# Kernel optimization log

Hardware: AMD Instinct MI355X
Metric: run time of the kernel (lower is better)

Reference implementation:

```python
import jax, jax.numpy as jnp
import numpy as np

EPS = 1e-9       # module's displacement/convergence epsilon
COS_EPS = 1e-8   # torch F.cosine_similarity eps (norms clamped at eps)
LN_EPS = 1e-5


def _safe_norm(sq):
    # sqrt with zero-safe gradient for exactly-zero (padded) vectors
    return jnp.where(sq > 0, jnp.sqrt(jnp.maximum(sq, 1e-30)), 0.0)


def _features(coords, n):
    """coords: [S, md] padded; n: true length (>=4). Returns [60] features."""
    S, md = coords.shape
    f32 = coords.dtype
    nf = n.astype(f32)
    idx_d = jnp.arange(S - 1)
    m = n - 1                       # number of valid deltas
    mf = m.astype(f32)
    dmask = idx_d < m
    dmaskf = dmask.astype(f32)

    deltas = (coords[1:] - coords[:-1]) * dmaskf[:, None]     # [S-1, md]
    dmags = _safe_norm(jnp.sum(deltas * deltas, axis=-1))      # [S-1]

    last = jnp.take(coords, n - 1, axis=0)
    total_disp = _safe_norm(jnp.sum((last - coords[0]) ** 2))
    path_len = jnp.sum(dmags)
    disp_ratio = total_disp / (path_len + EPS)
    n_steps_norm = nf / 10.0

    # consecutive cosine similarities / curvatures (valid count = n-2)
    na = jnp.maximum(dmags, COS_EPS)
    cos = jnp.sum(deltas[:-1] * deltas[1:], axis=-1) / (na[:-1] * na[1:])  # [S-2]
    idx_c = jnp.arange(S - 2)
    cmask = idx_c < (n - 2)
    cmaskf = cmask.astype(f32)
    ncf = (n - 2).astype(f32)
    curv = 1.0 - cos
    curv_m = jnp.where(cmask, curv, 0.0)
    mean_curv = jnp.sum(curv_m) / ncf
    max_curv = jnp.max(jnp.where(cmask, curv, -jnp.inf))
    min_curv = jnp.min(jnp.where(cmask, curv, jnp.inf))
    curv_var = jnp.sum(cmaskf * (curv - mean_curv) ** 2) / jnp.maximum(ncf - 1.0, 1.0)
    std_curv = jnp.where(ncf > 1.0, jnp.sqrt(jnp.maximum(curv_var, 1e-30)), 0.0)
    curv_range = max_curv - min_curv

    mean_cos = jnp.sum(jnp.where(cmask, cos, 0.0)) / ncf
    min_cos = jnp.min(jnp.where(cmask, cos, jnp.inf))
    dir_changes = jnp.sum(cmaskf * (cos < 0).astype(f32)) / jnp.maximum(ncf, 1.0)

    linearity = disp_ratio
    loop_score = 1.0 - total_disp / (path_len + EPS)

    half = m // 2
    fmaskf = (idx_d < half + 1).astype(f32)
    smaskf = ((idx_d >= half) & (idx_d < m)).astype(f32)
    first_half = jnp.sum(dmags * fmaskf) / (half + 1).astype(f32)
    second_half = jnp.sum(dmags * smaskf) / (m - half).astype(f32)
    convergence = (first_half - second_half) / (first_half + EPS)
    cascade = (second_half - first_half) / (first_half + EPS)

    # all-pairs cosine (the O(n^2) block) via one GEMM per sample
    cosmat = (deltas @ deltas.T) / (na[:, None] * na[None, :])  # [S-1, S-1]
    pmask = (idx_d[:, None] < idx_d[None, :]) & (idx_d[None, :] < m)
    npairs = mf * (mf - 1.0) / 2.0
    parallelism = jnp.sum(jnp.where(pmask, cosmat, 0.0)) / jnp.maximum(npairs, 1.0)

    mean_dm = path_len / mf
    dm_var = jnp.sum(dmaskf * (dmags - mean_dm) ** 2) / jnp.maximum(mf - 1.0, 1.0)
    std_dm = jnp.where(mf > 1.0, jnp.sqrt(jnp.maximum(dm_var, 1e-30)), 0.0)
    max_dm = jnp.max(jnp.where(dmask, dmags, -jnp.inf))
    jump = jnp.where(mean_dm > EPS, max_dm / mean_dm, 1.0)

    rmaskf = (jnp.arange(S) < n).astype(f32)
    cnt = nf * md
    mean_coord = jnp.sum(coords * rmaskf[:, None]) / cnt
    coord_var = jnp.sum(rmaskf[:, None] * (coords - mean_coord) ** 2) / (cnt - 1.0)
    std_coord = jnp.sqrt(jnp.maximum(coord_var, 1e-30))

    scalars = jnp.stack([
        total_disp, path_len, disp_ratio, n_steps_norm,
        mean_curv, max_curv, std_curv, curv_range,
        mean_cos, min_cos, dir_changes,
        linearity, loop_score, convergence, parallelism, jump, cascade,
        mean_dm, std_dm, mean_coord, std_coord,
    ])  # [21]
    padded_deltas = deltas[:3].reshape(-1)   # [30] (masked -> already zero-padded)
    padded_curvs = curv_m[:9]                # [9]
    return jnp.concatenate([scalars, padded_deltas, padded_curvs])  # [60]


def setup_inputs() -> dict:
    key = jax.random.key(0)
    ks = jax.random.split(key, 4)
    B, S, md, H = 32768, 48, 10, 48
    coords = jax.random.normal(ks[0], (B, S, md), dtype=jnp.float32)
    lengths = jax.random.randint(ks[1], (B,), 4, S + 1, dtype=jnp.int32)
    W = jax.random.normal(ks[2], (60, H), dtype=jnp.float32) * 0.1
    b = jax.random.normal(ks[3], (H,), dtype=jnp.float32) * 0.01
    ln_w = jnp.ones((H,), dtype=jnp.float32)
    ln_b = jnp.zeros((H,), dtype=jnp.float32)
    return {"coords": coords, "lengths": lengths, "W": W, "b": b, "ln_w": ln_w, "ln_b": ln_b}


def reference(coords, lengths, W, b, ln_w, ln_b):
    feats = jax.vmap(_features)(coords, lengths)          # [B, 60]
    h = feats @ W + b                                     # [B, 48]
    mu = jnp.mean(h, axis=-1, keepdims=True)
    var = jnp.mean((h - mu) ** 2, axis=-1, keepdims=True)
    h = (h - mu) / jnp.sqrt(var + LN_EPS) * ln_w + ln_b
    return jax.nn.gelu(h, approximate=False)              # dropout is identity at eval
```

## Files before the change

### kernel.cpp

```cpp
#include <hip/hip_runtime.h>
#include <math.h>

#define WPB 4

static __device__ __forceinline__ float frcp(float x){ return __builtin_amdgcn_rcpf(x); }
static __device__ __forceinline__ float fsq (float x){ return __builtin_amdgcn_sqrtf(x); }
static __device__ __forceinline__ float rld(float x, int l){
  return __uint_as_float(__builtin_amdgcn_readlane(__float_as_uint(x), l));
}

template<int CTRL, int RM>
static __device__ __forceinline__ float dppadd(float x){
  int t = __builtin_amdgcn_update_dpp(0, __float_as_int(x), CTRL, RM, 0xf, true);
  return x + __int_as_float(t);
}
template<int CTRL, int RM>
static __device__ __forceinline__ float dppmax(float x){
  int t = __builtin_amdgcn_update_dpp(__float_as_int(x), __float_as_int(x), CTRL, RM, 0xf, false);
  return fmaxf(x, __int_as_float(t));
}
template<int CTRL, int RM>
static __device__ __forceinline__ float dppmin(float x){
  int t = __builtin_amdgcn_update_dpp(__float_as_int(x), __float_as_int(x), CTRL, RM, 0xf, false);
  return fminf(x, __int_as_float(t));
}
static __device__ __forceinline__ float wsum63(float x){
  x = dppadd<0x111,0xf>(x); x = dppadd<0x112,0xf>(x);
  x = dppadd<0x114,0xf>(x); x = dppadd<0x118,0xf>(x);
  x = dppadd<0x142,0xa>(x); x = dppadd<0x143,0xc>(x);
  return x;
}
static __device__ __forceinline__ float wmax63(float x){
  x = dppmax<0x111,0xf>(x); x = dppmax<0x112,0xf>(x);
  x = dppmax<0x114,0xf>(x); x = dppmax<0x118,0xf>(x);
  x = dppmax<0x142,0xa>(x); x = dppmax<0x143,0xc>(x);
  return x;
}
static __device__ __forceinline__ float wmin63(float x){
  x = dppmin<0x111,0xf>(x); x = dppmin<0x112,0xf>(x);
  x = dppmin<0x114,0xf>(x); x = dppmin<0x118,0xf>(x);
  x = dppmin<0x142,0xa>(x); x = dppmin<0x143,0xc>(x);
  return x;
}

__global__ void transpose_w(const float* __restrict__ W, float* __restrict__ Wt){
  int idx = blockIdx.x * 256 + threadIdx.x;
  if (idx < 60 * 48) { int f = idx / 48, j = idx - f * 48; Wt[j * 60 + f] = W[idx]; }
}

template<bool USEWT>
__global__ __launch_bounds__(WPB * 64)
void traj_kernel(const float* __restrict__ coords,
                 const int* __restrict__ lengths,
                 const float* __restrict__ Wsrc,
                 const float* __restrict__ bias,
                 const float* __restrict__ lnw,
                 const float* __restrict__ lnb,
                 float* __restrict__ out, int B)
{
  const int i = threadIdx.x & 63;
  const int b = blockIdx.x * WPB + (threadIdx.x >> 6);
  if (b >= B) return;

  const int n = __builtin_amdgcn_readfirstlane(lengths[b]);
  const int m = n - 1;
  const int half = m >> 1;
  const float* cp = coords + (size_t)b * 480;

  const int r0 = (i < 47) ? i : 47;
  const int r1 = (i + 1 < 47) ? (i + 1) : 47;
  const int r2 = (i + 2 < 47) ? (i + 2) : 47;
  float c[10], cn[10], cnn[10];
  {
    const float2* p = reinterpret_cast<const float2*>(cp + r0 * 10);
#pragma unroll
    for (int k = 0; k < 5; ++k){ float2 v = p[k]; c[2*k]=v.x; c[2*k+1]=v.y; }
    p = reinterpret_cast<const float2*>(cp + r1 * 10);
#pragma unroll
    for (int k = 0; k < 5; ++k){ float2 v = p[k]; cn[2*k]=v.x; cn[2*k+1]=v.y; }
    p = reinterpret_cast<const float2*>(cp + r2 * 10);
#pragma unroll
    for (int k = 0; k < 5; ++k){ float2 v = p[k]; cnn[2*k]=v.x; cnn[2*k+1]=v.y; }
  }

  float d[10], dn[10];
  float dsq = 0.f, dsqn = 0.f, dot = 0.f;
#pragma unroll
  for (int k = 0; k < 10; ++k) {
    float a = cn[k] - c[k];   d[k]  = a;  dsq  = fmaf(a, a, dsq);
    float e = cnn[k] - cn[k]; dn[k] = e;  dsqn = fmaf(e, e, dsqn);
    dot = fmaf(a, e, dot);
  }
  const float sn   = (dsq  > 0.f) ? fsq(fmaxf(dsq,  1e-30f)) : 0.f;
  const float snn  = (dsqn > 0.f) ? fsq(fmaxf(dsqn, 1e-30f)) : 0.f;
  const float inv  = frcp(fmaxf(sn,  1e-8f));
  const float invn = frcp(fmaxf(snn, 1e-8f));

  const bool dact = (i < m);
  const float dm  = dact ? sn  : 0.f;
  const bool cact = (i < n - 2);
  const float cosv   = dot * inv * invn;
  const float cm     = cact ? cosv : 0.f;
  const float curv_m = cact ? (1.f - cosv) : 0.f;

  float csl = 0.f, cs2l = 0.f;
#pragma unroll
  for (int k = 0; k < 10; ++k) { csl += c[k]; cs2l = fmaf(c[k], c[k], cs2l); }
  const bool ract = (i < n);
  csl  = ract ? csl  : 0.f;
  cs2l = ract ? cs2l : 0.f;

  float tql = 0.f;
#pragma unroll
  for (int k = 0; k < 10; ++k) {
    float t = c[k] - rld(c[k], 0);
    tql = fmaf(t, t, tql);
  }
  const float tsq = rld(tql, m);
  const float total_disp = (tsq > 0.f) ? fsq(fmaxf(tsq, 1e-30f)) : 0.f;

  const float path_len = wsum63(dm);
  const float sum_dm2  = wsum63(dact ? dsq : 0.f);
  const float max_dm   = wmax63(dm);
  const float sum_f    = wsum63((i <= half) ? dm : 0.f);
  const float dm_half  = rld(dm, half);
  const float sum_cos  = wsum63(cm);
  const float sum_cos2 = wsum63(cm * cm);
  const float max_cos  = wmax63(cact ? cosv : -INFINITY);
  const float min_cos  = wmin63(cact ? cosv :  INFINITY);
  const float sum_ng   = wsum63((cact && cosv < 0.f) ? 1.f : 0.f);
  const float sum_c    = wsum63(csl);
  const float sum_c2   = wsum63(cs2l);
  const float invm = dact ? inv : 0.f;
  float Usq = 0.f;
#pragma unroll
  for (int k = 0; k < 10; ++k) {
    float Uk = wsum63(d[k] * invm);
    Usq = fmaf(Uk, Uk, Usq);
  }
  const float sum_uu = wsum63(dsq * invm * invm);

  const float EPSf = 1e-9f;
  const float nf = (float)n, mf = (float)m, ncf = (float)(n - 2);
  const float rncf = frcp(ncf);
  const float sum_s = path_len + dm_half - sum_f;
  const float disp_ratio = total_disp * frcp(path_len + EPSf);
  const float mean_cv = (ncf - sum_cos) * rncf;
  const float sum_cv2 = fmaf(-2.f, sum_cos, ncf) + sum_cos2;
  const float cv_var  = (sum_cv2 - ncf * mean_cv * mean_cv) * frcp(fmaxf(ncf - 1.f, 1.f));
  const float std_cv  = fsq(fmaxf(cv_var, 1e-30f));
  const float fh = sum_f * frcp((float)(half + 1));
  const float sh = sum_s * frcp((float)(m - half));
  const float conv = (fh - sh) * frcp(fh + EPSf);
  const float npairs = mf * (mf - 1.f) * 0.5f;
  const float par = (Usq - sum_uu) * 0.5f * frcp(npairs);
  const float mean_dm = path_len * frcp(mf);
  const float dm_var = (sum_dm2 - mf * mean_dm * mean_dm) * frcp(mf - 1.f);
  const float std_dm = fsq(fmaxf(dm_var, 1e-30f));
  const float jump = (mean_dm > EPSf) ? max_dm * frcp(mean_dm) : 1.f;
  const float cnt = nf * 10.f;
  const float mean_co = sum_c * frcp(cnt);
  const float co_var = (sum_c2 - cnt * mean_co * mean_co) * frcp(cnt - 1.f);
  const float std_co = fsq(fmaxf(co_var, 1e-30f));

  float feat[60];
  feat[0]  = rld(total_disp, 63);
  feat[1]  = rld(path_len, 63);
  feat[2]  = rld(disp_ratio, 63);
  feat[3]  = nf * 0.1f;
  feat[4]  = rld(mean_cv, 63);
  feat[5]  = 1.f - rld(min_cos, 63);
  feat[6]  = rld(std_cv, 63);
  feat[7]  = rld(max_cos - min_cos, 63);
  feat[8]  = rld(sum_cos * rncf, 63);
  feat[9]  = rld(min_cos, 63);
  feat[10] = rld(sum_ng * rncf, 63);
  feat[11] = feat[2];
  feat[12] = 1.f - feat[2];
  feat[13] = rld(conv, 63);
  feat[14] = rld(par, 63);
  feat[15] = rld(jump, 63);
  feat[16] = -feat[13];
  feat[17] = rld(mean_dm, 63);
  feat[18] = rld(std_dm, 63);
  feat[19] = rld(mean_co, 63);
  feat[20] = rld(std_co, 63);
#pragma unroll
  for (int k = 0; k < 10; ++k) feat[21 + k] = rld(d[k], 0);
#pragma unroll
  for (int k = 0; k < 10; ++k) feat[31 + k] = rld(d[k], 1);
#pragma unroll
  for (int k = 0; k < 10; ++k) feat[41 + k] = rld(d[k], 2);
#pragma unroll
  for (int r = 0; r < 9; ++r)  feat[51 + r] = rld(curv_m, r);

  const int jc = (i < 48) ? i : 47;
  float h = bias[jc];
  if (USEWT) {
    const float4* wr = reinterpret_cast<const float4*>(Wsrc + jc * 60);
#pragma unroll
    for (int t = 0; t < 15; ++t) {
      float4 w = wr[t];
      h = fmaf(feat[4*t+0], w.x, h);
      h = fmaf(feat[4*t+1], w.y, h);
      h = fmaf(feat[4*t+2], w.z, h);
      h = fmaf(feat[4*t+3], w.w, h);
    }
  } else {
#pragma unroll
    for (int f = 0; f < 60; ++f) h = fmaf(feat[f], Wsrc[f * 48 + jc], h);
  }

  const float hm = (i < 48) ? h : 0.f;
  const float s1 = rld(wsum63(hm), 63);
  const float s2 = rld(wsum63(hm * hm), 63);
  const float mu  = s1 * (1.f / 48.f);
  const float var = fmaf(-mu, mu, s2 * (1.f / 48.f));
  const float rstd = __builtin_amdgcn_rsqf(var + 1e-5f);

  if (i < 48) {
    float x = (h - mu) * rstd * lnw[i] + lnb[i];
    float x2 = x * x;
    float u  = 0.7978845608f * x * fmaf(0.044715f, x2, 1.f);
    float e  = __builtin_amdgcn_exp2f(u * 2.885390082f);
    float th = fmaf(-2.f, frcp(1.f + e), 1.f);
    out[(size_t)b * 48 + i] = 0.5f * x * (1.f + th);
  }
}

extern "C" void kernel_launch(void* const* d_in, const int* in_sizes, int n_in,
                              void* d_out, int out_size, void* d_ws, size_t ws_size,
                              hipStream_t stream)
{
  const float* coords = (const float*)d_in[0];
  const int*   lengths= (const int*)d_in[1];
  const float* W      = (const float*)d_in[2];
  const float* bias   = (const float*)d_in[3];
  const float* lnw    = (const float*)d_in[4];
  const float* lnb    = (const float*)d_in[5];
  float* out = (float*)d_out;

  const int B = in_sizes[1];
  const int blocks = (B + WPB - 1) / WPB;

  if (ws_size >= (size_t)(60 * 48 * sizeof(float))) {
    float* Wt = (float*)d_ws;
    transpose_w<<<12, 256, 0, stream>>>(W, Wt);
    traj_kernel<true><<<blocks, WPB * 64, 0, stream>>>(coords, lengths, Wt, bias, lnw, lnb, out, B);
  } else {
    traj_kernel<false><<<blocks, WPB * 64, 0, stream>>>(coords, lengths, W, bias, lnw, lnb, out, B);
  }
}
```

Before: 132.1 us.

## Split into feature kernel with 4 threads per trajectory and separate MLP kernel

Replaces the one-wavefront-per-trajectory fused kernel with two kernels. A feature kernel assigns four threads to each trajectory, each scanning twelve rows serially and combining partial sums with quad DPP reductions, then writes 60 features to workspace. A separate MLP kernel reads those features and applies the linear layer, LayerNorm and GELU. The goal is to cut the heavy cross-lane reduction overhead and idle lanes of the old layout. The cost is a global round trip for the features and strided per-thread loads. The fallback branch now uses workspace regardless of its size, which can overflow it.

```diff
diff --git a/kernel.cpp b/kernel.cpp
--- a/kernel.cpp
+++ b/kernel.cpp
@@ -1,7 +1,5 @@
 #include <hip/hip_runtime.h>
 #include <math.h>
-
-#define WPB 4
 
 static __device__ __forceinline__ float frcp(float x){ return __builtin_amdgcn_rcpf(x); }
 static __device__ __forceinline__ float fsq (float x){ return __builtin_amdgcn_sqrtf(x); }
@@ -9,20 +7,29 @@
   return __uint_as_float(__builtin_amdgcn_readlane(__float_as_uint(x), l));
 }
 
+template<int CTRL>
+static __device__ __forceinline__ float qaddd(float x){
+  int t = __builtin_amdgcn_update_dpp(0, __float_as_int(x), CTRL, 0xf, 0xf, true);
+  return x + __int_as_float(t);
+}
+template<int CTRL>
+static __device__ __forceinline__ float qmaxd(float x){
+  int t = __builtin_amdgcn_update_dpp(__float_as_int(x), __float_as_int(x), CTRL, 0xf, 0xf, false);
+  return fmaxf(x, __int_as_float(t));
+}
+template<int CTRL>
+static __device__ __forceinline__ float qmind(float x){
+  int t = __builtin_amdgcn_update_dpp(__float_as_int(x), __float_as_int(x), CTRL, 0xf, 0xf, false);
+  return fminf(x, __int_as_float(t));
+}
+static __device__ __forceinline__ float qsum(float x){ return qaddd<0x4E>(qaddd<0xB1>(x)); }
+static __device__ __forceinline__ float qmax(float x){ return qmaxd<0x4E>(qmaxd<0xB1>(x)); }
+static __device__ __forceinline__ float qmin(float x){ return qmind<0x4E>(qmind<0xB1>(x)); }
+
 template<int CTRL, int RM>
 static __device__ __forceinline__ float dppadd(float x){
   int t = __builtin_amdgcn_update_dpp(0, __float_as_int(x), CTRL, RM, 0xf, true);
   return x + __int_as_float(t);
-}
-template<int CTRL, int RM>
-static __device__ __forceinline__ float dppmax(float x){
-  int t = __builtin_amdgcn_update_dpp(__float_as_int(x), __float_as_int(x), CTRL, RM, 0xf, false);
-  return fmaxf(x, __int_as_float(t));
-}
-template<int CTRL, int RM>
-static __device__ __forceinline__ float dppmin(float x){
-  int t = __builtin_amdgcn_update_dpp(__float_as_int(x), __float_as_int(x), CTRL, RM, 0xf, false);
-  return fminf(x, __int_as_float(t));
 }
 static __device__ __forceinline__ float wsum63(float x){
   x = dppadd<0x111,0xf>(x); x = dppadd<0x112,0xf>(x);
@@ -30,201 +37,229 @@
   x = dppadd<0x142,0xa>(x); x = dppadd<0x143,0xc>(x);
   return x;
 }
-static __device__ __forceinline__ float wmax63(float x){
-  x = dppmax<0x111,0xf>(x); x = dppmax<0x112,0xf>(x);
-  x = dppmax<0x114,0xf>(x); x = dppmax<0x118,0xf>(x);
-  x = dppmax<0x142,0xa>(x); x = dppmax<0x143,0xc>(x);
-  return x;
-}
-static __device__ __forceinline__ float wmin63(float x){
-  x = dppmin<0x111,0xf>(x); x = dppmin<0x112,0xf>(x);
-  x = dppmin<0x114,0xf>(x); x = dppmin<0x118,0xf>(x);
-  x = dppmin<0x142,0xa>(x); x = dppmin<0x143,0xc>(x);
-  return x;
-}
 
 __global__ void transpose_w(const float* __restrict__ W, float* __restrict__ Wt){
   int idx = blockIdx.x * 256 + threadIdx.x;
   if (idx < 60 * 48) { int f = idx / 48, j = idx - f * 48; Wt[j * 60 + f] = W[idx]; }
 }
 
-template<bool USEWT>
-__global__ __launch_bounds__(WPB * 64)
-void traj_kernel(const float* __restrict__ coords,
+__global__ __launch_bounds__(256)
+void feat_kernel(const float* __restrict__ coords,
                  const int* __restrict__ lengths,
-                 const float* __restrict__ Wsrc,
-                 const float* __restrict__ bias,
-                 const float* __restrict__ lnw,
-                 const float* __restrict__ lnb,
-                 float* __restrict__ out, int B)
+                 float* __restrict__ feats, int B)
 {
-  const int i = threadIdx.x & 63;
-  const int b = blockIdx.x * WPB + (threadIdx.x >> 6);
-  if (b >= B) return;
-
-  const int n = __builtin_amdgcn_readfirstlane(lengths[b]);
+  const int t    = blockIdx.x * 256 + threadIdx.x;
+  const int traj = t >> 2;
+  const int p    = t & 3;
+  if (traj >= B) return;
+
+  const int n = lengths[traj];
   const int m = n - 1;
   const int half = m >> 1;
-  const float* cp = coords + (size_t)b * 480;
-
-  const int r0 = (i < 47) ? i : 47;
-  const int r1 = (i + 1 < 47) ? (i + 1) : 47;
-  const int r2 = (i + 2 < 47) ? (i + 2) : 47;
-  float c[10], cn[10], cnn[10];
+  const float* cp = coords + (size_t)traj * 480;
+  float* fb = feats + (size_t)traj * 60;
+  const int base = p * 12;
+
+  float prev[10];
   {
-    const float2* p = reinterpret_cast<const float2*>(cp + r0 * 10);
-#pragma unroll
-    for (int k = 0; k < 5; ++k){ float2 v = p[k]; c[2*k]=v.x; c[2*k+1]=v.y; }
-    p = reinterpret_cast<const float2*>(cp + r1 * 10);
-#pragma unroll
-    for (int k = 0; k < 5; ++k){ float2 v = p[k]; cn[2*k]=v.x; cn[2*k+1]=v.y; }
-    p = reinterpret_cast<const float2*>(cp + r2 * 10);
-#pragma unroll
-    for (int k = 0; k < 5; ++k){ float2 v = p[k]; cnn[2*k]=v.x; cnn[2*k+1]=v.y; }
-  }
-
-  float d[10], dn[10];
-  float dsq = 0.f, dsqn = 0.f, dot = 0.f;
-#pragma unroll
-  for (int k = 0; k < 10; ++k) {
-    float a = cn[k] - c[k];   d[k]  = a;  dsq  = fmaf(a, a, dsq);
-    float e = cnn[k] - cn[k]; dn[k] = e;  dsqn = fmaf(e, e, dsqn);
-    dot = fmaf(a, e, dot);
-  }
-  const float sn   = (dsq  > 0.f) ? fsq(fmaxf(dsq,  1e-30f)) : 0.f;
-  const float snn  = (dsqn > 0.f) ? fsq(fmaxf(dsqn, 1e-30f)) : 0.f;
-  const float inv  = frcp(fmaxf(sn,  1e-8f));
-  const float invn = frcp(fmaxf(snn, 1e-8f));
-
-  const bool dact = (i < m);
-  const float dm  = dact ? sn  : 0.f;
-  const bool cact = (i < n - 2);
-  const float cosv   = dot * inv * invn;
-  const float cm     = cact ? cosv : 0.f;
-  const float curv_m = cact ? (1.f - cosv) : 0.f;
-
-  float csl = 0.f, cs2l = 0.f;
-#pragma unroll
-  for (int k = 0; k < 10; ++k) { csl += c[k]; cs2l = fmaf(c[k], c[k], cs2l); }
-  const bool ract = (i < n);
-  csl  = ract ? csl  : 0.f;
-  cs2l = ract ? cs2l : 0.f;
-
-  float tql = 0.f;
-#pragma unroll
-  for (int k = 0; k < 10; ++k) {
-    float t = c[k] - rld(c[k], 0);
-    tql = fmaf(t, t, tql);
-  }
-  const float tsq = rld(tql, m);
-  const float total_disp = (tsq > 0.f) ? fsq(fmaxf(tsq, 1e-30f)) : 0.f;
-
-  const float path_len = wsum63(dm);
-  const float sum_dm2  = wsum63(dact ? dsq : 0.f);
-  const float max_dm   = wmax63(dm);
-  const float sum_f    = wsum63((i <= half) ? dm : 0.f);
-  const float dm_half  = rld(dm, half);
-  const float sum_cos  = wsum63(cm);
-  const float sum_cos2 = wsum63(cm * cm);
-  const float max_cos  = wmax63(cact ? cosv : -INFINITY);
-  const float min_cos  = wmin63(cact ? cosv :  INFINITY);
-  const float sum_ng   = wsum63((cact && cosv < 0.f) ? 1.f : 0.f);
-  const float sum_c    = wsum63(csl);
-  const float sum_c2   = wsum63(cs2l);
-  const float invm = dact ? inv : 0.f;
+    const float2* pp = reinterpret_cast<const float2*>(cp + base * 10);
+#pragma unroll
+    for (int k = 0; k < 5; ++k){ float2 v = pp[k]; prev[2*k]=v.x; prev[2*k+1]=v.y; }
+  }
+
+  float d_prev[10];
+#pragma unroll
+  for (int k = 0; k < 10; ++k) d_prev[k] = 0.f;
+  float inv_prev = 0.f;
+
+  float path=0.f, dm2=0.f, mxdm=0.f, sf=0.f, ss=0.f, uu=0.f;
+  float scos=0.f, scos2=0.f, sng=0.f, csl=0.f, cs2=0.f;
+  float mxc=-INFINITY, mnc=INFINITY;
+  float uk[10];
+#pragma unroll
+  for (int k = 0; k < 10; ++k) uk[k] = 0.f;
+
+#pragma unroll
+  for (int dj = 0; dj < 13; ++dj) {
+    const int j = base + dj;
+
+    if (dj < 12 && j < n) {
+      float t1 = 0.f, t2 = 0.f;
+#pragma unroll
+      for (int k = 0; k < 10; ++k) { t1 += prev[k]; t2 = fmaf(prev[k], prev[k], t2); }
+      csl += t1; cs2 += t2;
+    }
+
+    const int rn = (j + 1 < 47) ? (j + 1) : 47;
+    float nx[10];
+    {
+      const float2* pp = reinterpret_cast<const float2*>(cp + rn * 10);
+#pragma unroll
+      for (int k = 0; k < 5; ++k){ float2 v = pp[k]; nx[2*k]=v.x; nx[2*k+1]=v.y; }
+    }
+
+    float d[10]; float dsq = 0.f, dot = 0.f;
+#pragma unroll
+    for (int k = 0; k < 10; ++k) {
+      float a = nx[k] - prev[k];
+      d[k] = a;
+      dsq = fmaf(a, a, dsq);
+      dot = fmaf(d_prev[k], a, dot);
+    }
+    const float sn  = (dsq > 0.f) ? fsq(fmaxf(dsq, 1e-30f)) : 0.f;
+    const float inv = frcp(fmaxf(sn, 1e-8f));
+
+    if (dj < 12) {
+      const bool act = j < m;
+      const float dm = act ? sn : 0.f;
+      path += dm;
+      dm2  += act ? dsq : 0.f;
+      mxdm  = fmaxf(mxdm, dm);
+      sf   += (j <= half) ? dm : 0.f;
+      ss   += (j >= half) ? dm : 0.f;
+      const float im = act ? inv : 0.f;
+#pragma unroll
+      for (int k = 0; k < 10; ++k) uk[k] = fmaf(d[k], im, uk[k]);
+      uu = fmaf(dsq * im, im, uu);
+      if (p == 0 && dj < 3) {
+#pragma unroll
+        for (int k = 0; k < 10; ++k) fb[21 + dj * 10 + k] = d[k];
+      }
+    }
+
+    if (dj >= 1) {
+      const int jc = j - 1;
+      const bool ca = jc < (n - 2);
+      const float cosv = dot * inv_prev * inv;
+      const float cm = ca ? cosv : 0.f;
+      scos  += cm;
+      scos2  = fmaf(cm, cm, scos2);
+      mxc    = fmaxf(mxc, ca ? cosv : -INFINITY);
+      mnc    = fminf(mnc, ca ? cosv :  INFINITY);
+      sng   += (ca && cosv < 0.f) ? 1.f : 0.f;
+      if (p == 0 && dj <= 9) fb[51 + jc] = ca ? (1.f - cosv) : 0.f;
+    }
+
+#pragma unroll
+    for (int k = 0; k < 10; ++k) { prev[k] = nx[k]; d_prev[k] = d[k]; }
+    inv_prev = inv;
+  }
+
+  float tq = 0.f;
+  if (m >= base && m < base + 12) {
+    const float2* p0 = reinterpret_cast<const float2*>(cp);
+    const float2* pm = reinterpret_cast<const float2*>(cp + m * 10);
+#pragma unroll
+    for (int k = 0; k < 5; ++k) {
+      float2 a = p0[k], z = pm[k];
+      float dx = z.x - a.x, dy = z.y - a.y;
+      tq = fmaf(dx, dx, fmaf(dy, dy, tq));
+    }
+  }
+
+  path = qsum(path);  dm2 = qsum(dm2);   mxdm = qmax(mxdm);
+  sf   = qsum(sf);    ss  = qsum(ss);    uu   = qsum(uu);
+  scos = qsum(scos);  scos2 = qsum(scos2); sng = qsum(sng);
+  mxc  = qmax(mxc);   mnc = qmin(mnc);
+  csl  = qsum(csl);   cs2 = qsum(cs2);   tq   = qsum(tq);
   float Usq = 0.f;
 #pragma unroll
-  for (int k = 0; k < 10; ++k) {
-    float Uk = wsum63(d[k] * invm);
-    Usq = fmaf(Uk, Uk, Usq);
-  }
-  const float sum_uu = wsum63(dsq * invm * invm);
+  for (int k = 0; k < 10; ++k) { float Uk = qsum(uk[k]); Usq = fmaf(Uk, Uk, Usq); }
 
   const float EPSf = 1e-9f;
   const float nf = (float)n, mf = (float)m, ncf = (float)(n - 2);
   const float rncf = frcp(ncf);
-  const float sum_s = path_len + dm_half - sum_f;
-  const float disp_ratio = total_disp * frcp(path_len + EPSf);
-  const float mean_cv = (ncf - sum_cos) * rncf;
-  const float sum_cv2 = fmaf(-2.f, sum_cos, ncf) + sum_cos2;
+  const float total_disp = (tq > 0.f) ? fsq(fmaxf(tq, 1e-30f)) : 0.f;
+  const float disp_ratio = total_disp * frcp(path + EPSf);
+  const float mean_cv = (ncf - scos) * rncf;
+  const float sum_cv2 = fmaf(-2.f, scos, ncf) + scos2;
   const float cv_var  = (sum_cv2 - ncf * mean_cv * mean_cv) * frcp(fmaxf(ncf - 1.f, 1.f));
   const float std_cv  = fsq(fmaxf(cv_var, 1e-30f));
-  const float fh = sum_f * frcp((float)(half + 1));
-  const float sh = sum_s * frcp((float)(m - half));
+  const float fh = sf * frcp((float)(half + 1));
+  const float sh = ss * frcp((float)(m - half));
   const float conv = (fh - sh) * frcp(fh + EPSf);
   const float npairs = mf * (mf - 1.f) * 0.5f;
-  const float par = (Usq - sum_uu) * 0.5f * frcp(npairs);
-  const float mean_dm = path_len * frcp(mf);
-  const float dm_var = (sum_dm2 - mf * mean_dm * mean_dm) * frcp(mf - 1.f);
+  const float par = (Usq - uu) * 0.5f * frcp(fmaxf(npairs, 1.f));
+  const float mean_dm = path * frcp(mf);
+  const float dm_var = (dm2 - mf * mean_dm * mean_dm) * frcp(mf - 1.f);
   const float std_dm = fsq(fmaxf(dm_var, 1e-30f));
-  const float jump = (mean_dm > EPSf) ? max_dm * frcp(mean_dm) : 1.f;
+  const float jump = (mean_dm > EPSf) ? mxdm * frcp(mean_dm) : 1.f;
   const float cnt = nf * 10.f;
-  const float mean_co = sum_c * frcp(cnt);
-  const float co_var = (sum_c2 - cnt * mean_co * mean_co) * frcp(cnt - 1.f);
+  const float mean_co = csl * frcp(cnt);
+  const float co_var = (cs2 - cnt * mean_co * mean_co) * frcp(cnt - 1.f);
   const float std_co = fsq(fmaxf(co_var, 1e-30f));
 
-  float feat[60];
-  feat[0]  = rld(total_disp, 63);
-  feat[1]  = rld(path_len, 63);
-  feat[2]  = rld(disp_ratio, 63);
-  feat[3]  = nf * 0.1f;
-  feat[4]  = rld(mean_cv, 63);
-  feat[5]  = 1.f - rld(min_cos, 63);
-  feat[6]  = rld(std_cv, 63);
-  feat[7]  = rld(max_cos - min_cos, 63);
-  feat[8]  = rld(sum_cos * rncf, 63);
-  feat[9]  = rld(min_cos, 63);
-  feat[10] = rld(sum_ng * rncf, 63);
-  feat[11] = feat[2];
-  feat[12] = 1.f - feat[2];
-  feat[13] = rld(conv, 63);
-  feat[14] = rld(par, 63);
-  feat[15] = rld(jump, 63);
-  feat[16] = -feat[13];
-  feat[17] = rld(mean_dm, 63);
-  feat[18] = rld(std_dm, 63);
-  feat[19] = rld(mean_co, 63);
-  feat[20] = rld(std_co, 63);
-#pragma unroll
-  for (int k = 0; k < 10; ++k) feat[21 + k] = rld(d[k], 0);
-#pragma unroll
-  for (int k = 0; k < 10; ++k) feat[31 + k] = rld(d[k], 1);
-#pragma unroll
-  for (int k = 0; k < 10; ++k) feat[41 + k] = rld(d[k], 2);
-#pragma unroll
-  for (int r = 0; r < 9; ++r)  feat[51 + r] = rld(curv_m, r);
-
-  const int jc = (i < 48) ? i : 47;
+  if (p == 0) {
+    fb[0]  = total_disp;
+    fb[1]  = path;
+    fb[2]  = disp_ratio;
+    fb[3]  = nf * 0.1f;
+    fb[4]  = mean_cv;
+    fb[5]  = 1.f - mnc;
+    fb[6]  = std_cv;
+    fb[7]  = mxc - mnc;
+    fb[8]  = scos * rncf;
+    fb[9]  = mnc;
+    fb[10] = sng * rncf;
+    fb[11] = disp_ratio;
+    fb[12] = 1.f - disp_ratio;
+    fb[13] = conv;
+    fb[14] = par;
+    fb[15] = jump;
+    fb[16] = -conv;
+    fb[17] = mean_dm;
+    fb[18] = std_dm;
+    fb[19] = mean_co;
+    fb[20] = std_co;
+  }
+}
+
+__global__ __launch_bounds__(256)
+void mlp_kernel(const float* __restrict__ feats,
+                const float* __restrict__ Wt,
+                const float* __restrict__ bias,
+                const float* __restrict__ lnw,
+                const float* __restrict__ lnb,
+                float* __restrict__ out, int B)
+{
+  const int lane = threadIdx.x & 63;
+  const int b = blockIdx.x * 4 + (threadIdx.x >> 6);
+  if (b >= B) return;
+
+  const float* fp = feats + (size_t)b * 60;
+  float f[60];
+#pragma unroll
+  for (int q = 0; q < 15; ++q) {
+    float4 v = reinterpret_cast<const float4*>(fp)[q];
+    f[4*q] = v.x; f[4*q+1] = v.y; f[4*q+2] = v.z; f[4*q+3] = v.w;
+  }
+
+  const int jc = (lane < 48) ? lane : 47;
   float h = bias[jc];
-  if (USEWT) {
-    const float4* wr = reinterpret_cast<const float4*>(Wsrc + jc * 60);
-#pragma unroll
-    for (int t = 0; t < 15; ++t) {
-      float4 w = wr[t];
-      h = fmaf(feat[4*t+0], w.x, h);
-      h = fmaf(feat[4*t+1], w.y, h);
-      h = fmaf(feat[4*t+2], w.z, h);
-      h = fmaf(feat[4*t+3], w.w, h);
-    }
-  } else {
-#pragma unroll
-    for (int f = 0; f < 60; ++f) h = fmaf(feat[f], Wsrc[f * 48 + jc], h);
-  }
-
-  const float hm = (i < 48) ? h : 0.f;
+  const float4* wr = reinterpret_cast<const float4*>(Wt + jc * 60);
+#pragma unroll
+  for (int q = 0; q < 15; ++q) {
+    float4 w = wr[q];
+    h = fmaf(f[4*q+0], w.x, h);
+    h = fmaf(f[4*q+1], w.y, h);
+    h = fmaf(f[4*q+2], w.z, h);
+    h = fmaf(f[4*q+3], w.w, h);
+  }
+
+  const float hm = (lane < 48) ? h : 0.f;
   const float s1 = rld(wsum63(hm), 63);
   const float s2 = rld(wsum63(hm * hm), 63);
   const float mu  = s1 * (1.f / 48.f);
   const float var = fmaf(-mu, mu, s2 * (1.f / 48.f));
   const float rstd = __builtin_amdgcn_rsqf(var + 1e-5f);
 
-  if (i < 48) {
-    float x = (h - mu) * rstd * lnw[i] + lnb[i];
+  if (lane < 48) {
+    float x = (h - mu) * rstd * lnw[lane] + lnb[lane];
     float x2 = x * x;
     float u  = 0.7978845608f * x * fmaf(0.044715f, x2, 1.f);
     float e  = __builtin_amdgcn_exp2f(u * 2.885390082f);
     float th = fmaf(-2.f, frcp(1.f + e), 1.f);
-    out[(size_t)b * 48 + i] = 0.5f * x * (1.f + th);
+    out[(size_t)b * 48 + lane] = 0.5f * x * (1.f + th);
   }
 }
 
@@ -241,13 +276,19 @@
   float* out = (float*)d_out;
 
   const int B = in_sizes[1];
-  const int blocks = (B + WPB - 1) / WPB;
-
-  if (ws_size >= (size_t)(60 * 48 * sizeof(float))) {
-    float* Wt = (float*)d_ws;
+  const size_t need = (size_t)(2880 + (size_t)B * 60) * sizeof(float);
+
+  if (ws_size >= need) {
+    float* Wt    = (float*)d_ws;
+    float* feats = (float*)d_ws + 2880;
     transpose_w<<<12, 256, 0, stream>>>(W, Wt);
-    traj_kernel<true><<<blocks, WPB * 64, 0, stream>>>(coords, lengths, Wt, bias, lnw, lnb, out, B);
+    feat_kernel<<<(B * 4 + 255) / 256, 256, 0, stream>>>(coords, lengths, feats, B);
+    mlp_kernel<<<(B + 3) / 4, 256, 0, stream>>>(feats, Wt, bias, lnw, lnb, out, B);
   } else {
-    traj_kernel<false><<<blocks, WPB * 64, 0, stream>>>(coords, lengths, W, bias, lnw, lnb, out, B);
-  }
-}
+    float* Wt    = (float*)d_ws;
+    float* feats = (float*)d_ws + 2880;
+    transpose_w<<<12, 256, 0, stream>>>(W, Wt);
+    feat_kernel<<<(B * 4 + 255) / 256, 256, 0, stream>>>(coords, lengths, feats, B);
+    mlp_kernel<<<(B + 3) / 4, 256, 0, stream>>>(feats, Wt, bias, lnw, lnb, out, B);
+  }
+}
```

Result: slower. 167.8 us (+27.0%).
